# Kernel tuning notes

Hardware: AMD Instinct MI355X
Metric: run time of the kernel (lower is better)

Reference implementation:

```python
import jax, jax.numpy as jnp
import numpy as np

N = 100000   # num nodes
E = 1600000  # num edges (avg degree 16)
D = 64       # feature dim (in_size == out_size, proj unused in forward_dglsp)
EPS = 1e-12  # F.normalize eps


def setup_inputs() -> dict:
    key = jax.random.key(0)
    k1, k2, k3 = jax.random.split(key, 3)
    H = jax.random.normal(k1, (N, D), dtype=jnp.float32)
    row = jnp.sort(jax.random.randint(k2, (E,), 0, N, dtype=jnp.int64))  # dst (CSR-like)
    col = jax.random.randint(k3, (E,), 0, N, dtype=jnp.int64)            # src
    return {"H": H, "row": row, "col": col, "num_nodes": N}


def reference(H, row, col, num_nodes):
    # F.normalize(H, p=2, dim=1): divide by max(||h||, eps)
    norm = jnp.sqrt(jnp.sum(H * H, axis=1, keepdims=True))
    Hn = H / jnp.maximum(norm, EPS)

    # bsddmm(A, Hn, Hn.T): cosine-sim score per edge (r, c) = Hn[r] . Hn[c]
    scores = jnp.sum(Hn[row] * Hn[col], axis=1)  # [E]

    # edge softmax per destination row (dglsp softmax along last dim)
    m = jax.ops.segment_max(scores, row, num_segments=num_nodes)  # [N]
    e = jnp.exp(scores - m[row])
    s = jax.ops.segment_sum(e, row, num_segments=num_nodes)       # [N]
    attn = e / s[row]                                             # [E]

    # bspmm(attn, H): out[r] = sum over edges (r,c) attn * H[c]
    out = jax.ops.segment_sum(attn[:, None] * H[col], row, num_segments=num_nodes)
    return out  # [N, D]
```

## Files before the change

### kernel.cpp

```cpp
#include <hip/hip_runtime.h>
#include <math.h>

#define D 64
#define EPS 1e-12f

__global__ void norm_kernel(const float4* __restrict__ H4,
                            float* __restrict__ inv_norm, int N) {
    int tid = blockIdx.x * blockDim.x + threadIdx.x;
    int r   = tid >> 4;
    int sub = tid & 15;
    if (r >= N) return;
    float4 v = H4[(size_t)r * 16 + sub];
    float ss = v.x * v.x + v.y * v.y + v.z * v.z + v.w * v.w;
    ss += __shfl_xor(ss, 1, 64);
    ss += __shfl_xor(ss, 2, 64);
    ss += __shfl_xor(ss, 4, 64);
    ss += __shfl_xor(ss, 8, 64);
    if (sub == 0) inv_norm[r] = 1.0f / fmaxf(sqrtf(ss), EPS);
}

__global__ void rowptr_kernel(const int* __restrict__ row,
                              int* __restrict__ row_ptr, int E, int N) {
    int e = blockIdx.x * blockDim.x + threadIdx.x;
    if (e >= E) return;
    int cur  = row[e];
    int prev = (e == 0) ? -1 : row[e - 1];
    for (int r = prev + 1; r <= cur; ++r) row_ptr[r] = e;
    if (e == E - 1) {
        for (int r = cur + 1; r <= N; ++r) row_ptr[r] = E;
    }
}

__global__ __launch_bounds__(256) void agnn_kernel(
    const float* __restrict__ H,
    const float* __restrict__ inv_norm,
    const int* __restrict__ row_ptr,
    const int* __restrict__ col,
    float* __restrict__ out, int N) {
    int wid  = (blockIdx.x * blockDim.x + threadIdx.x) >> 6;
    int lane = threadIdx.x & 63;
    if (wid >= N) return;
    int g   = lane >> 4;
    int sub = lane & 15;

    int start = row_ptr[wid];
    int end   = row_ptr[wid + 1];

    const float4* H4 = (const float4*)H;
    float4 hr = H4[(size_t)wid * 16 + sub];
    float inr = inv_norm[wid];
    hr.x *= inr; hr.y *= inr; hr.z *= inr; hr.w *= inr;

    float  m = -INFINITY, l = 0.0f;
    float4 acc = {0.0f, 0.0f, 0.0f, 0.0f};

    int e = start + g;
    int   c_cur = 0;
    float in_cur = 0.0f;
    float4 hc_cur = {0, 0, 0, 0};
    if (e < end) {
        c_cur  = col[e];
        in_cur = inv_norm[c_cur];
        hc_cur = H4[(size_t)c_cur * 16 + sub];
    }

    for (; e < end; e += 4) {
        int    c_n = 0;
        float  in_n = 0.0f;
        float4 hc_n = {0, 0, 0, 0};
        if (e + 4 < end) {
            c_n  = col[e + 4];
            in_n = inv_norm[c_n];
            hc_n = H4[(size_t)c_n * 16 + sub];
        }

        float s = hr.x * hc_cur.x + hr.y * hc_cur.y +
                  hr.z * hc_cur.z + hr.w * hc_cur.w;
        s += __shfl_xor(s, 1, 64);
        s += __shfl_xor(s, 2, 64);
        s += __shfl_xor(s, 4, 64);
        s += __shfl_xor(s, 8, 64);
        s *= in_cur;

        float m_new  = fmaxf(m, s);
        float scale  = __expf(m - m_new);
        float p      = __expf(s - m_new);
        l = l * scale + p;
        acc.x = acc.x * scale + p * hc_cur.x;
        acc.y = acc.y * scale + p * hc_cur.y;
        acc.z = acc.z * scale + p * hc_cur.z;
        acc.w = acc.w * scale + p * hc_cur.w;
        m = m_new;

        hc_cur = hc_n; in_cur = in_n; c_cur = c_n;
    }

    #pragma unroll
    for (int off = 16; off <= 32; off <<= 1) {
        float  m_o = __shfl_xor(m, off, 64);
        float  l_o = __shfl_xor(l, off, 64);
        float4 a_o;
        a_o.x = __shfl_xor(acc.x, off, 64);
        a_o.y = __shfl_xor(acc.y, off, 64);
        a_o.z = __shfl_xor(acc.z, off, 64);
        a_o.w = __shfl_xor(acc.w, off, 64);
        float m_new = fmaxf(m, m_o);
        float sa = (m   == -INFINITY) ? 0.0f : __expf(m   - m_new);
        float sb = (m_o == -INFINITY) ? 0.0f : __expf(m_o - m_new);
        l = l * sa + l_o * sb;
        acc.x = acc.x * sa + a_o.x * sb;
        acc.y = acc.y * sa + a_o.y * sb;
        acc.z = acc.z * sa + a_o.z * sb;
        acc.w = acc.w * sa + a_o.w * sb;
        m = m_new;
    }

    if (g == 0) {
        float invl = (l > 0.0f) ? 1.0f / l : 0.0f;
        float4 o;
        o.x = acc.x * invl; o.y = acc.y * invl;
        o.z = acc.z * invl; o.w = acc.w * invl;
        ((float4*)out)[(size_t)wid * 16 + sub] = o;
    }
}

extern "C" void kernel_launch(void* const* d_in, const int* in_sizes, int n_in,
                              void* d_out, int out_size, void* d_ws, size_t ws_size,
                              hipStream_t stream) {
    const float* H   = (const float*)d_in[0];
    const int*   row = (const int*)d_in[1];
    const int*   col = (const int*)d_in[2];
    float*       out = (float*)d_out;

    int N = in_sizes[0] / D;
    int E = in_sizes[1];

    float* inv_norm = (float*)d_ws;
    int*   row_ptr  = (int*)((char*)d_ws + (size_t)N * sizeof(float));

    norm_kernel<<<(N * 16 + 255) / 256, 256, 0, stream>>>((const float4*)H, inv_norm, N);
    rowptr_kernel<<<(E + 255) / 256, 256, 0, stream>>>(row, row_ptr, E, N);
    agnn_kernel<<<(N + 3) / 4, 256, 0, stream>>>(H, inv_norm, row_ptr, col, out, N);
}
```

Baseline: 157.1 us.

## Drop online-softmax max tracking, unroll edge loop by two, fuse prep kernels

Cosine scores are bounded in [-1,1], so the kernel drops the running max and rescaling and accumulates exp(s) directly. The merge across lane groups becomes a plain sum. The edge loop now handles two edges per group per iteration with a two-deep prefetch, giving more memory-level parallelism. The norm and row_ptr kernels are merged into one launch. This relies on the bounded score range for numerical safety and adds register pressure.

Measured after the change: 149.8 us. -4.7%, faster.

```diff
diff --git a/kernel.cpp b/kernel.cpp
--- a/kernel.cpp
+++ b/kernel.cpp
@@ -4,30 +4,28 @@
 #define D 64
 #define EPS 1e-12f
 
-__global__ void norm_kernel(const float4* __restrict__ H4,
-                            float* __restrict__ inv_norm, int N) {
-    int tid = blockIdx.x * blockDim.x + threadIdx.x;
-    int r   = tid >> 4;
-    int sub = tid & 15;
-    if (r >= N) return;
-    float4 v = H4[(size_t)r * 16 + sub];
-    float ss = v.x * v.x + v.y * v.y + v.z * v.z + v.w * v.w;
-    ss += __shfl_xor(ss, 1, 64);
-    ss += __shfl_xor(ss, 2, 64);
-    ss += __shfl_xor(ss, 4, 64);
-    ss += __shfl_xor(ss, 8, 64);
-    if (sub == 0) inv_norm[r] = 1.0f / fmaxf(sqrtf(ss), EPS);
-}
-
-__global__ void rowptr_kernel(const int* __restrict__ row,
-                              int* __restrict__ row_ptr, int E, int N) {
-    int e = blockIdx.x * blockDim.x + threadIdx.x;
-    if (e >= E) return;
-    int cur  = row[e];
-    int prev = (e == 0) ? -1 : row[e - 1];
-    for (int r = prev + 1; r <= cur; ++r) row_ptr[r] = e;
-    if (e == E - 1) {
-        for (int r = cur + 1; r <= N; ++r) row_ptr[r] = E;
+__global__ void prep_kernel(const float4* __restrict__ H4,
+                            float* __restrict__ inv_norm,
+                            const int* __restrict__ row,
+                            int* __restrict__ row_ptr, int N, int E) {
+    int t = blockIdx.x * blockDim.x + threadIdx.x;
+    if (t < N * 16) {
+        int r = t >> 4, sub = t & 15;
+        float4 v = H4[(size_t)r * 16 + sub];
+        float ss = v.x * v.x + v.y * v.y + v.z * v.z + v.w * v.w;
+        ss += __shfl_xor(ss, 1, 64);
+        ss += __shfl_xor(ss, 2, 64);
+        ss += __shfl_xor(ss, 4, 64);
+        ss += __shfl_xor(ss, 8, 64);
+        if (sub == 0) inv_norm[r] = 1.0f / fmaxf(sqrtf(ss), EPS);
+    }
+    if (t < E) {
+        int cur  = row[t];
+        int prev = (t == 0) ? -1 : row[t - 1];
+        for (int r = prev + 1; r <= cur; ++r) row_ptr[r] = t;
+        if (t == E - 1) {
+            for (int r = cur + 1; r <= N; ++r) row_ptr[r] = E;
+        }
     }
 }
 
@@ -51,68 +49,46 @@
     float inr = inv_norm[wid];
     hr.x *= inr; hr.y *= inr; hr.z *= inr; hr.w *= inr;
 
-    float  m = -INFINITY, l = 0.0f;
+    float  l = 0.0f;
     float4 acc = {0.0f, 0.0f, 0.0f, 0.0f};
 
     int e = start + g;
-    int   c_cur = 0;
-    float in_cur = 0.0f;
-    float4 hc_cur = {0, 0, 0, 0};
-    if (e < end) {
-        c_cur  = col[e];
-        in_cur = inv_norm[c_cur];
-        hc_cur = H4[(size_t)c_cur * 16 + sub];
-    }
+    float4 h0 = {0, 0, 0, 0}, h1 = {0, 0, 0, 0};
+    float in0 = 0.0f, in1 = 0.0f, v0 = 0.0f, v1 = 0.0f;
+    if (e < end)     { int c = col[e];     in0 = inv_norm[c]; h0 = H4[(size_t)c * 16 + sub]; v0 = 1.0f; }
+    if (e + 4 < end) { int c = col[e + 4]; in1 = inv_norm[c]; h1 = H4[(size_t)c * 16 + sub]; v1 = 1.0f; }
 
-    for (; e < end; e += 4) {
-        int    c_n = 0;
-        float  in_n = 0.0f;
-        float4 hc_n = {0, 0, 0, 0};
-        if (e + 4 < end) {
-            c_n  = col[e + 4];
-            in_n = inv_norm[c_n];
-            hc_n = H4[(size_t)c_n * 16 + sub];
-        }
+    for (; e < end; e += 8) {
+        float4 nh0 = {0, 0, 0, 0}, nh1 = {0, 0, 0, 0};
+        float nin0 = 0.0f, nin1 = 0.0f, nv0 = 0.0f, nv1 = 0.0f;
+        if (e + 8  < end) { int c = col[e + 8];  nin0 = inv_norm[c]; nh0 = H4[(size_t)c * 16 + sub]; nv0 = 1.0f; }
+        if (e + 12 < end) { int c = col[e + 12]; nin1 = inv_norm[c]; nh1 = H4[(size_t)c * 16 + sub]; nv1 = 1.0f; }
 
-        float s = hr.x * hc_cur.x + hr.y * hc_cur.y +
-                  hr.z * hc_cur.z + hr.w * hc_cur.w;
-        s += __shfl_xor(s, 1, 64);
-        s += __shfl_xor(s, 2, 64);
-        s += __shfl_xor(s, 4, 64);
-        s += __shfl_xor(s, 8, 64);
-        s *= in_cur;
+        float s0 = hr.x * h0.x + hr.y * h0.y + hr.z * h0.z + hr.w * h0.w;
+        float s1 = hr.x * h1.x + hr.y * h1.y + hr.z * h1.z + hr.w * h1.w;
+        s0 += __shfl_xor(s0, 1, 64);  s1 += __shfl_xor(s1, 1, 64);
+        s0 += __shfl_xor(s0, 2, 64);  s1 += __shfl_xor(s1, 2, 64);
+        s0 += __shfl_xor(s0, 4, 64);  s1 += __shfl_xor(s1, 4, 64);
+        s0 += __shfl_xor(s0, 8, 64);  s1 += __shfl_xor(s1, 8, 64);
 
-        float m_new  = fmaxf(m, s);
-        float scale  = __expf(m - m_new);
-        float p      = __expf(s - m_new);
-        l = l * scale + p;
-        acc.x = acc.x * scale + p * hc_cur.x;
-        acc.y = acc.y * scale + p * hc_cur.y;
-        acc.z = acc.z * scale + p * hc_cur.z;
-        acc.w = acc.w * scale + p * hc_cur.w;
-        m = m_new;
+        float p0 = v0 * __expf(s0 * in0);
+        float p1 = v1 * __expf(s1 * in1);
+        l += p0 + p1;
+        acc.x += p0 * h0.x + p1 * h1.x;
+        acc.y += p0 * h0.y + p1 * h1.y;
+        acc.z += p0 * h0.z + p1 * h1.z;
+        acc.w += p0 * h0.w + p1 * h1.w;
 
-        hc_cur = hc_n; in_cur = in_n; c_cur = c_n;
+        h0 = nh0; h1 = nh1; in0 = nin0; in1 = nin1; v0 = nv0; v1 = nv1;
     }
 
     #pragma unroll
     for (int off = 16; off <= 32; off <<= 1) {
-        float  m_o = __shfl_xor(m, off, 64);
-        float  l_o = __shfl_xor(l, off, 64);
-        float4 a_o;
-        a_o.x = __shfl_xor(acc.x, off, 64);
-        a_o.y = __shfl_xor(acc.y, off, 64);
-        a_o.z = __shfl_xor(acc.z, off, 64);
-        a_o.w = __shfl_xor(acc.w, off, 64);
-        float m_new = fmaxf(m, m_o);
-        float sa = (m   == -INFINITY) ? 0.0f : __expf(m   - m_new);
-        float sb = (m_o == -INFINITY) ? 0.0f : __expf(m_o - m_new);
-        l = l * sa + l_o * sb;
-        acc.x = acc.x * sa + a_o.x * sb;
-        acc.y = acc.y * sa + a_o.y * sb;
-        acc.z = acc.z * sa + a_o.z * sb;
-        acc.w = acc.w * sa + a_o.w * sb;
-        m = m_new;
+        l     += __shfl_xor(l, off, 64);
+        acc.x += __shfl_xor(acc.x, off, 64);
+        acc.y += __shfl_xor(acc.y, off, 64);
+        acc.z += __shfl_xor(acc.z, off, 64);
+        acc.w += __shfl_xor(acc.w, off, 64);
     }
 
     if (g == 0) {
@@ -138,7 +114,8 @@
     float* inv_norm = (float*)d_ws;
     int*   row_ptr  = (int*)((char*)d_ws + (size_t)N * sizeof(float));
 
-    norm_kernel<<<(N * 16 + 255) / 256, 256, 0, stream>>>((const float4*)H, inv_norm, N);
-    rowptr_kernel<<<(E + 255) / 256, 256, 0, stream>>>(row, row_ptr, E, N);
+    int prep_threads = (N * 16 > E) ? N * 16 : E;
+    prep_kernel<<<(prep_threads + 255) / 256, 256, 0, stream>>>(
+        (const float4*)H, inv_norm, row, row_ptr, N, E);
     agnn_kernel<<<(N + 3) / 4, 256, 0, stream>>>(H, inv_norm, row_ptr, col, out, N);
 }
```
